# Optimization experiments

Measured on AMD Instinct MI355X. Metric: run time of the kernel, lower is better.

The kernel has to match this reference:

```python
import jax, jax.numpy as jnp
import numpy as np

RX = 49
R = 1.0
ANGLES = [-10.0, 0.0, 10.0]


def _make_kernels(rx, r, angles_deg):
    # same construction as the torch __init__
    angles = np.rad2deg(np.arctan(r * np.tan(np.deg2rad(np.asarray(angles_deg, np.float64)))))
    ks = []
    for A in angles:
        lval = np.arange(rx) - rx // 2
        lval = np.round(lval * np.tan(np.deg2rad(A))).astype(np.int32)
        ry = (lval.max() - lval.min()) // 2 * 2 + 1
        i, _ = np.meshgrid(np.arange(ry), np.arange(rx))
        i = i - ry // 2
        k = (i == lval[:, None]).astype(np.float32)[None, None]  # [1,1,rx,ry], one nonzero per row
        ks.append(k)
    return ks

_KERNELS = [jnp.asarray(k) for k in _make_kernels(RX, R, ANGLES)]
_PADS = [(int(k.shape[2]) // 2, int(k.shape[3]) // 2) for k in _KERNELS]  # (pc, pr)


def _boxfilter(x, k, pc, pr):
    # torch.conv2d(F.pad(x,(pr,pr,pc,pc)), k) == cross-correlation with symmetric zero pad
    return jax.lax.conv_general_dilated(x, k, (1, 1), ((pc, pc), (pr, pr)),
                                        dimension_numbers=('NCHW', 'OIHW', 'NCHW'))


def _reflect(x, size):
    # PyTorch reflection padding for align_corners=True: reflect about [0, size-1]
    span = size - 1
    if span <= 0:
        return jnp.zeros_like(x)
    ax = jnp.abs(x)
    extra = jnp.mod(ax, span)
    flips = jnp.floor(ax / span)
    out = jnp.where(jnp.mod(flips, 2.0) == 0.0, extra, span - extra)
    return jnp.clip(out, 0.0, span)


def _grid_sample(x, grid):
    # bilinear, padding_mode='reflection', align_corners=True; x:[B,C,H,W], grid:[B,Hg,Wg,2]
    B, C, H, W = x.shape
    gx = _reflect((grid[..., 0] + 1.0) * 0.5 * (W - 1), W)
    gy = _reflect((grid[..., 1] + 1.0) * 0.5 * (H - 1), H)
    x0 = jnp.floor(gx)
    y0 = jnp.floor(gy)
    wx = gx - x0
    wy = gy - y0
    xi0 = jnp.clip(x0, 0, W - 1).astype(jnp.int32)
    yi0 = jnp.clip(y0, 0, H - 1).astype(jnp.int32)
    xi1 = jnp.clip(x0 + 1.0, 0, W - 1).astype(jnp.int32)
    yi1 = jnp.clip(y0 + 1.0, 0, H - 1).astype(jnp.int32)
    gather = jax.vmap(lambda img, yi, xi: img[:, yi, xi])  # [B,C,Hg,Wg]
    v00 = gather(x, yi0, xi0)
    v01 = gather(x, yi0, xi1)
    v10 = gather(x, yi1, xi0)
    v11 = gather(x, yi1, xi1)
    wx = wx[:, None]  # [B,1,Hg,Wg] broadcast over channel
    wy = wy[:, None]
    return (v00 * (1 - wx) * (1 - wy) + v01 * wx * (1 - wy)
            + v10 * (1 - wx) * wy + v11 * wx * wy)


def setup_inputs() -> dict:
    key = jax.random.key(0)
    k1, k2, k3, k4 = jax.random.split(key, 4)
    B, H, W = 1, 2048, 2048
    X = jax.random.uniform(k1, (B, 1, H, W), jnp.float32)
    y = jax.random.uniform(k2, (B, 1, H, W), jnp.float32)
    hX = jax.random.normal(k3, (B, 1, H, W), jnp.float32)
    coor = jax.random.uniform(k4, (B, H, W, 2), jnp.float32, minval=-1.0, maxval=1.0)
    return {"X": X, "y": y, "hX": hX, "coor": coor}


def reference(X, y, hX, coor):
    # N: normalization = boxfilter of ones (computed once per shape in torch; recomputed here)
    N = [_boxfilter(jnp.ones_like(X), k, pc, pr) for k, (pc, pr) in zip(_KERNELS, _PADS)]
    X0 = X
    Xc = X
    for (k, (pc, pr)), Ni in zip(zip(_KERNELS, _PADS), N):
        b = _boxfilter(y - Xc, k, pc, pr) / Ni
        b = _boxfilter(b, k, pc, pr) / Ni
        Xc = Xc + b
    return _grid_sample(Xc - X0, coor) + hX
```

## Files before the change

kernel.cpp:

```cpp
#include <hip/hip_runtime.h>
#include <hip/hip_fp16.h>

static constexpr int HH = 2048;
static constexpr int WW = 2048;
static constexpr int PADT = 24;
static constexpr int PADL = 8;
static constexpr int SW   = WW + 2 * PADL;
static constexpr int PROWS = HH + 2 * PADT;
static constexpr size_t PadElems = (size_t)PROWS * SW;
static constexpr int RSP = 8;
static constexpr int RV = 16;

__device__ constexpr int CS[9] = {-24,-19,-14,-8,-2, 3, 9,15,20};
__device__ constexpr int CE[9] = {-20,-15, -9,-3, 2, 8,14,19,24};
__device__ constexpr int CO[9] = { -4, -3, -2,-1, 0, 1, 2, 3, 4};

union U32H2 { unsigned u; __half2 h; };
__device__ __forceinline__ __half2 u2h(unsigned u) { U32H2 x; x.u = u; return x.h; }
__device__ __forceinline__ unsigned h2u(__half2 h) { U32H2 x; x.h = h; return x.u; }

__device__ __forceinline__ void swz_s2(int& bx, int& by) {
  const int bid = blockIdx.x;
  const int xcd = bid & 7, i = bid >> 3;
  by = xcd * 32 + (i & 31);
  bx = i >> 5;
}
__device__ __forceinline__ void swz_v(int& bx, int& by) {
  const int bid = blockIdx.x;
  const int xcd = bid & 7, i = bid >> 3;
  by = xcd * 16 + (i & 15);
  bx = i >> 4;
}

template<int SS, int EE, int OO, int NROWS>
__device__ __forceinline__ void seg2p(const __half* __restrict__ tp, int h0, int w2,
                                      __half2* __restrict__ acc) {
  constexpr int NR = EE - SS;
  constexpr bool EVEN = ((OO & 1) == 0);
  const size_t st = SW / 2;
  const unsigned* p = (const unsigned*)(tp + (size_t)(h0 + SS + PADT) * SW +
                                        (w2 + PADL + (EVEN ? OO : OO - 1)));
  unsigned ring[NR];
  __half2 s = u2h(0u);
#pragma unroll
  for (int k = 0; k < NR; ++k) {
    unsigned u;
    if constexpr (EVEN) { u = p[k * st]; }
    else { const unsigned ul = p[k * st], ur = p[k * st + 1]; u = (ul >> 16) | (ur << 16); }
    ring[k] = u;
    s = __hadd2(s, u2h(u));
  }
#pragma unroll
  for (int r = 0; r < NROWS; ++r) {
    unsigned u;
    if constexpr (EVEN) { u = p[(NR + r) * st]; }
    else { const unsigned ul = p[(NR + r) * st], ur = p[(NR + r) * st + 1]; u = (ul >> 16) | (ur << 16); }
    const __half2 v = u2h(u);
    acc[r] = __hadd2(acc[r], __hadd2(s, v));
    s = __hadd2(s, __hsub2(v, u2h(ring[r % NR])));
    ring[r % NR] = u;
  }
}

template<int SGN, int NROWS>
__device__ __forceinline__ void filt_slant2p(const __half* __restrict__ tp, int h0, int w2,
                                             __half2* __restrict__ acc) {
#pragma unroll
  for (int r = 0; r < NROWS; ++r) acc[r] = u2h(0u);
  seg2p<-24, -20, -4 * SGN, NROWS>(tp, h0, w2, acc);
  seg2p<-19, -15, -3 * SGN, NROWS>(tp, h0, w2, acc);
  seg2p<-14,  -9, -2 * SGN, NROWS>(tp, h0, w2, acc);
  seg2p< -8,  -3, -1 * SGN, NROWS>(tp, h0, w2, acc);
  seg2p< -2,   2,  0      , NROWS>(tp, h0, w2, acc);
  seg2p<  3,   8,  1 * SGN, NROWS>(tp, h0, w2, acc);
  seg2p<  9,  14,  2 * SGN, NROWS>(tp, h0, w2, acc);
  seg2p< 15,  19,  3 * SGN, NROWS>(tp, h0, w2, acc);
  seg2p< 20,  24,  4 * SGN, NROWS>(tp, h0, w2, acc);
}

template<int A>
__device__ __forceinline__ float rcpcnt(int h, int w) {
  if (h >= 24 && h <= 2023 && w >= 4 && w <= 2043) return 1.0f / 49.0f;
  int cnt = 0;
  const int sgn = (A == 0) ? -1 : 1;
#pragma unroll
  for (int j = 0; j < 9; ++j) {
    const int ww = w + sgn * CO[j];
    const int ov = min(h + CE[j], HH - 1) - max(h + CS[j], 0) + 1;
    if (ww >= 0 && ww < WW && ov > 0) cnt += ov;
  }
  return 1.0f / (float)cnt;
}

__device__ __forceinline__ float rcpcnt1(int h) {
  return 1.0f / (float)(min(h + 24, HH - 1) - max(h - 24, 0) + 1);
}

template<int A>
__global__ __launch_bounds__(256) void passA(const __half* __restrict__ tcur,
                                             __half* __restrict__ bp) {
  int bx, by; swz_s2(bx, by);
  const int w2 = (bx * 256 + threadIdx.x) * 2;
  const int h0 = by * RSP;
  __half2 acc[RSP];
  filt_slant2p<(A == 0) ? -1 : 1, RSP>(tcur, h0, w2, acc);
#pragma unroll
  for (int r = 0; r < RSP; ++r) {
    const int h = h0 + r;
    const float2 f = __half22float2(acc[r]);
    *(unsigned*)(bp + (size_t)(h + PADT) * SW + (w2 + PADL)) =
        h2u(__floats2half2_rn(f.x * rcpcnt<A>(h, w2), f.y * rcpcnt<A>(h, w2 + 1)));
  }
}

template<int A>
__global__ __launch_bounds__(256) void passB(const __half* __restrict__ bp,
                                             __half* __restrict__ tcur) {
  int bx, by; swz_s2(bx, by);
  const int w2 = (bx * 256 + threadIdx.x) * 2;
  const int h0 = by * RSP;
  __half2 acc[RSP];
  filt_slant2p<(A == 0) ? -1 : 1, RSP>(bp, h0, w2, acc);
#pragma unroll
  for (int r = 0; r < RSP; ++r) {
    const int h = h0 + r;
    unsigned* o = (unsigned*)(tcur + (size_t)(h + PADT) * SW + (w2 + PADL));
    const float2 cur = __half22float2(u2h(*o));
    const float2 f = __half22float2(acc[r]);
    *o = h2u(__floats2half2_rn(cur.x - f.x * rcpcnt<A>(h, w2),
                               cur.y - f.y * rcpcnt<A>(h, w2 + 1)));
  }
}

template<int A>
__global__ __launch_bounds__(256) void passBF(const __half* __restrict__ bp,
                                              __half* __restrict__ tcur,
                                              const __half* __restrict__ t0h,
                                              unsigned int* __restrict__ scaleU) {
  int bx, by; swz_s2(bx, by);
  const int w2 = (bx * 256 + threadIdx.x) * 2;
  const int h0 = by * RSP;
  __half2 acc[RSP];
  filt_slant2p<(A == 0) ? -1 : 1, RSP>(bp, h0, w2, acc);
  float m = 0.0f;
#pragma unroll
  for (int r = 0; r < RSP; ++r) {
    const int h = h0 + r;
    const float2 t0 = __half22float2(u2h(*(const unsigned*)(t0h + (size_t)h * WW + w2)));
    unsigned* o = (unsigned*)(tcur + (size_t)(h + PADT) * SW + (w2 + PADL));
    const float2 cur = __half22float2(u2h(*o));
    const float2 f = __half22float2(acc[r]);
    const float rx = t0.x - cur.x + f.x * rcpcnt<A>(h, w2);
    const float ry = t0.y - cur.y + f.y * rcpcnt<A>(h, w2 + 1);
    *o = h2u(__floats2half2_rn(rx, ry));
    m = fmaxf(m, fmaxf(fabsf(rx), fabsf(ry)));
  }
#pragma unroll
  for (int off = 32; off >= 1; off >>= 1) m = fmaxf(m, __shfl_xor(m, off));
  __shared__ float red[4];
  if ((threadIdx.x & 63) == 0) red[threadIdx.x >> 6] = m;
  __syncthreads();
  if (threadIdx.x == 0) {
    const float bm = fmaxf(fmaxf(red[0], red[1]), fmaxf(red[2], red[3]));
    atomicMax(scaleU, __float_as_uint(bm));
  }
}

__global__ __launch_bounds__(256) void passA1v(const __half* __restrict__ tcur,
                                               __half* __restrict__ bp) {
  int bx, by; swz_v(bx, by);
  const int w2 = (bx * 256 + threadIdx.x) * 2;
  const int h0 = by * RV;
  const size_t st = SW / 2;
  const unsigned* p = (const unsigned*)(tcur + (size_t)(h0 - 24 + PADT) * SW + (w2 + PADL));
  __half2 s = u2h(0u);
#pragma unroll
  for (int k = 0; k < 48; ++k) s = __hadd2(s, u2h(p[k * st]));
#pragma unroll
  for (int r = 0; r < RV; ++r) {
    const int h = h0 + r;
    const __half2 vin = u2h(p[(48 + r) * st]);
    const float2 f = __half22float2(__hadd2(s, vin));
    const float rc = rcpcnt1(h);
    *(unsigned*)(bp + (size_t)(h + PADT) * SW + (w2 + PADL)) =
        h2u(__floats2half2_rn(f.x * rc, f.y * rc));
    s = __hadd2(s, __hsub2(vin, u2h(p[r * st])));
  }
}

__global__ __launch_bounds__(256) void passB1v(const __half* __restrict__ bp,
                                               __half* __restrict__ tcur) {
  int bx, by; swz_v(bx, by);
  const int w2 = (bx * 256 + threadIdx.x) * 2;
  const int h0 = by * RV;
  const size_t st = SW / 2;
  const unsigned* p = (const unsigned*)(bp + (size_t)(h0 - 24 + PADT) * SW + (w2 + PADL));
  __half2 s = u2h(0u);
#pragma unroll
  for (int k = 0; k < 48; ++k) s = __hadd2(s, u2h(p[k * st]));
#pragma unroll
  for (int r = 0; r < RV; ++r) {
    const int h = h0 + r;
    const __half2 vin = u2h(p[(48 + r) * st]);
    const float2 f = __half22float2(__hadd2(s, vin));
    const float rc = rcpcnt1(h);
    unsigned* o = (unsigned*)(tcur + (size_t)(h + PADT) * SW + (w2 + PADL));
    const float2 cur = __half22float2(u2h(*o));
    *o = h2u(__floats2half2_rn(cur.x - f.x * rc, cur.y - f.y * rc));
    s = __hadd2(s, __hsub2(vin, u2h(p[r * st])));
  }
}

__global__ __launch_bounds__(256) void quantV8(const __half* __restrict__ tcur,
                                               const unsigned int* __restrict__ scaleU,
                                               unsigned long long* __restrict__ V8) {
  const int i = blockIdx.x * 256 + threadIdx.x;
  const int s = i >> 10, x2 = (i & 1023) * 2;
  const float mg = __uint_as_float(*scaleU);
  const float inv = (mg > 0.0f) ? 127.0f / mg : 0.0f;
  const unsigned* base = (const unsigned*)(tcur + (size_t)(8 * s + PADT) * SW + (x2 + PADL));
  const size_t st = SW / 2;
  unsigned long long va = 0, vb = 0;
#pragma unroll
  for (int j = 0; j < 8; ++j) {
    const float2 f = __half22float2(u2h(base[(size_t)j * st]));
    const int qa = min(max((int)rintf(f.x * inv), -127), 127);
    const int qb = min(max((int)rintf(f.y * inv), -127), 127);
    va |= (unsigned long long)(unsigned char)(qa & 0xff) << (8 * j);
    vb |= (unsigned long long)(unsigned char)(qb & 0xff) << (8 * j);
  }
  unsigned long long* o = V8 + (size_t)s * WW + x2;
  o[0] = va; o[1] = vb;
}

__global__ __launch_bounds__(64) void zeropad(__half* __restrict__ tp, __half* __restrict__ bp,
                                              unsigned int* __restrict__ scaleU) {
  if (blockIdx.x == 0 && blockIdx.y == 0 && threadIdx.x == 0) *scaleU = 0u;
  __half* buf = blockIdx.y ? bp : tp;
  const int row = blockIdx.x;
  __half* r = buf + (size_t)row * SW;
  const __half z = __float2half(0.0f);
  if (row < PADT || row >= PADT + HH) {
    for (int c = threadIdx.x; c < SW; c += 64) r[c] = z;
  } else if (threadIdx.x < PADL) {
    r[threadIdx.x] = z;
    r[PADL + WW + threadIdx.x] = z;
  }
}

__global__ __launch_bounds__(256) void sub2pad(const float* __restrict__ y,
                                               const float* __restrict__ X,
                                               __half* __restrict__ tcur,
                                               __half* __restrict__ t0h) {
  const int i = blockIdx.x * 256 + threadIdx.x;
  const int p = i * 4;
  const int h = p >> 11, w = p & (WW - 1);
  const float4 Y = ((const float4*)y)[i];
  const float4 Xv = ((const float4*)X)[i];
  union { __half2 h2; unsigned u; } a, b;
  a.h2 = __floats2half2_rn(Y.x - Xv.x, Y.y - Xv.y);
  b.h2 = __floats2half2_rn(Y.z - Xv.z, Y.w - Xv.w);
  uint2 o; o.x = a.u; o.y = b.u;
  *(uint2*)(tcur + (size_t)(h + PADT) * SW + (w + PADL)) = o;
  *(uint2*)(t0h + (size_t)p) = o;
}

__global__ __launch_bounds__(256) void gather_k(const unsigned long long* __restrict__ V8,
                                                const unsigned int* __restrict__ scaleU,
                                                const unsigned long long* __restrict__ coorU,
                                                const float* __restrict__ hX,
                                                float* __restrict__ out) {
  const int i = blockIdx.x * 256 + threadIdx.x;
  const unsigned long long cu = __builtin_nontemporal_load(&coorU[i]);
  union { unsigned long long u; float f[2]; } cc; cc.u = cu;
  const float gx = fminf(fmaxf((cc.f[0] + 1.0f) * 0.5f * (float)(WW - 1), 0.0f), (float)(WW - 1));
  const float gy = fminf(fmaxf((cc.f[1] + 1.0f) * 0.5f * (float)(HH - 1), 0.0f), (float)(HH - 1));
  const float x0 = floorf(gx), y0 = floorf(gy);
  const float wx = gx - x0, wy = gy - y0;
  const int xi0 = min(max((int)x0, 0), WW - 1);
  const int xi1 = min(xi0 + 1, WW - 1);
  const int yi0 = min(max((int)y0, 0), HH - 1);
  const int yi1 = min(max((int)(y0 + 1.0f), 0), HH - 1);
  const int s0 = yi0 >> 3, s1 = yi1 >> 3;
  const int j0 = (yi0 & 7) * 8, j1 = (yi1 & 7) * 8;
  const unsigned long long c00 = V8[(size_t)s0 * WW + xi0];
  const unsigned long long c01 = V8[(size_t)s0 * WW + xi1];
  unsigned long long c10 = c00, c11 = c01;
  if (s1 != s0) {
    c10 = V8[(size_t)s1 * WW + xi0];
    c11 = V8[(size_t)s1 * WW + xi1];
  }
  const float v00 = (float)(signed char)(c00 >> j0);
  const float v01 = (float)(signed char)(c01 >> j0);
  const float v10 = (float)(signed char)(c10 >> j1);
  const float v11 = (float)(signed char)(c11 >> j1);
  const float sc = __uint_as_float(*scaleU) * (1.0f / 127.0f);
  const float hx = __builtin_nontemporal_load(&hX[i]);
  const float bil = v00 * (1.0f - wx) * (1.0f - wy) + v01 * wx * (1.0f - wy) +
                    v10 * (1.0f - wx) * wy + v11 * wx * wy;
  __builtin_nontemporal_store(bil * sc + hx, &out[i]);
}

extern "C" void kernel_launch(void* const* d_in, const int* in_sizes, int n_in,
                              void* d_out, int out_size, void* d_ws, size_t ws_size,
                              hipStream_t stream) {
  const float* X    = (const float*)d_in[0];
  const float* y    = (const float*)d_in[1];
  const float* hX   = (const float*)d_in[2];
  const float* coor = (const float*)d_in[3];
  float* out = (float*)d_out;

  __half* tcur = (__half*)d_ws;
  __half* bp   = tcur + PadElems;
  __half* t0h  = bp + PadElems;
  unsigned long long* V8 = (unsigned long long*)(t0h + (size_t)HH * WW);
  unsigned int* scaleU = (unsigned int*)(V8 + (size_t)(HH / 8) * WW);

  const int n = HH * WW;
  const int sblocks = (WW / 512) * (HH / RSP);
  const int vblocks = (WW / 512) * (HH / RV);

  zeropad<<<dim3(PROWS, 2, 1), 64, 0, stream>>>(tcur, bp, scaleU);
  sub2pad<<<(n / 4) / 256, 256, 0, stream>>>(y, X, tcur, t0h);

  passA<0><<<sblocks, 256, 0, stream>>>(tcur, bp);
  passB<0><<<sblocks, 256, 0, stream>>>(bp, tcur);
  passA1v<<<vblocks, 256, 0, stream>>>(tcur, bp);
  passB1v<<<vblocks, 256, 0, stream>>>(bp, tcur);
  passA<2><<<sblocks, 256, 0, stream>>>(tcur, bp);
  passBF<2><<<sblocks, 256, 0, stream>>>(bp, tcur, t0h, scaleU);

  quantV8<<<((HH / 8) * (WW / 2)) / 256, 256, 0, stream>>>(tcur, scaleU, V8);
  gather_k<<<n / 256, 256, 0, stream>>>(V8, scaleU, (const unsigned long long*)coor, hX, out);
}
```

Measured before the change: 147.3 us.

## Use overlapping 7-row int8 packs so bilinear gather needs two loads

```diff
diff --git a/kernel.cpp b/kernel.cpp
--- a/kernel.cpp
+++ b/kernel.cpp
@@ -8,8 +8,9 @@
 static constexpr int SW   = WW + 2 * PADL;
 static constexpr int PROWS = HH + 2 * PADT;
 static constexpr size_t PadElems = (size_t)PROWS * SW;
-static constexpr int RSP = 8;
+static constexpr int RSP = 16;
 static constexpr int RV = 16;
+static constexpr int NG = 293;
 
 __device__ constexpr int CS[9] = {-24,-19,-14,-8,-2, 3, 9,15,20};
 __device__ constexpr int CE[9] = {-20,-15, -9,-3, 2, 8,14,19,24};
@@ -19,13 +20,7 @@
 __device__ __forceinline__ __half2 u2h(unsigned u) { U32H2 x; x.u = u; return x.h; }
 __device__ __forceinline__ unsigned h2u(__half2 h) { U32H2 x; x.h = h; return x.u; }
 
-__device__ __forceinline__ void swz_s2(int& bx, int& by) {
-  const int bid = blockIdx.x;
-  const int xcd = bid & 7, i = bid >> 3;
-  by = xcd * 32 + (i & 31);
-  bx = i >> 5;
-}
-__device__ __forceinline__ void swz_v(int& bx, int& by) {
+__device__ __forceinline__ void swz_f(int& bx, int& by) {
   const int bid = blockIdx.x;
   const int xcd = bid & 7, i = bid >> 3;
   by = xcd * 16 + (i & 15);
@@ -99,7 +94,7 @@
 template<int A>
 __global__ __launch_bounds__(256) void passA(const __half* __restrict__ tcur,
                                              __half* __restrict__ bp) {
-  int bx, by; swz_s2(bx, by);
+  int bx, by; swz_f(bx, by);
   const int w2 = (bx * 256 + threadIdx.x) * 2;
   const int h0 = by * RSP;
   __half2 acc[RSP];
@@ -116,7 +111,7 @@
 template<int A>
 __global__ __launch_bounds__(256) void passB(const __half* __restrict__ bp,
                                              __half* __restrict__ tcur) {
-  int bx, by; swz_s2(bx, by);
+  int bx, by; swz_f(bx, by);
   const int w2 = (bx * 256 + threadIdx.x) * 2;
   const int h0 = by * RSP;
   __half2 acc[RSP];
@@ -137,7 +132,7 @@
                                               __half* __restrict__ tcur,
                                               const __half* __restrict__ t0h,
                                               unsigned int* __restrict__ scaleU) {
-  int bx, by; swz_s2(bx, by);
+  int bx, by; swz_f(bx, by);
   const int w2 = (bx * 256 + threadIdx.x) * 2;
   const int h0 = by * RSP;
   __half2 acc[RSP];
@@ -168,7 +163,7 @@
 
 __global__ __launch_bounds__(256) void passA1v(const __half* __restrict__ tcur,
                                                __half* __restrict__ bp) {
-  int bx, by; swz_v(bx, by);
+  int bx, by; swz_f(bx, by);
   const int w2 = (bx * 256 + threadIdx.x) * 2;
   const int h0 = by * RV;
   const size_t st = SW / 2;
@@ -190,7 +185,7 @@
 
 __global__ __launch_bounds__(256) void passB1v(const __half* __restrict__ bp,
                                                __half* __restrict__ tcur) {
-  int bx, by; swz_v(bx, by);
+  int bx, by; swz_f(bx, by);
   const int w2 = (bx * 256 + threadIdx.x) * 2;
   const int h0 = by * RV;
   const size_t st = SW / 2;
@@ -211,14 +206,14 @@
   }
 }
 
-__global__ __launch_bounds__(256) void quantV8(const __half* __restrict__ tcur,
-                                               const unsigned int* __restrict__ scaleU,
-                                               unsigned long long* __restrict__ V8) {
+__global__ __launch_bounds__(256) void quantV8s7(const __half* __restrict__ tcur,
+                                                 const unsigned int* __restrict__ scaleU,
+                                                 unsigned long long* __restrict__ V8) {
   const int i = blockIdx.x * 256 + threadIdx.x;
   const int s = i >> 10, x2 = (i & 1023) * 2;
   const float mg = __uint_as_float(*scaleU);
   const float inv = (mg > 0.0f) ? 127.0f / mg : 0.0f;
-  const unsigned* base = (const unsigned*)(tcur + (size_t)(8 * s + PADT) * SW + (x2 + PADL));
+  const unsigned* base = (const unsigned*)(tcur + (size_t)(7 * s + PADT) * SW + (x2 + PADL));
   const size_t st = SW / 2;
   unsigned long long va = 0, vb = 0;
 #pragma unroll
@@ -233,36 +228,38 @@
   o[0] = va; o[1] = vb;
 }
 
-__global__ __launch_bounds__(64) void zeropad(__half* __restrict__ tp, __half* __restrict__ bp,
-                                              unsigned int* __restrict__ scaleU) {
-  if (blockIdx.x == 0 && blockIdx.y == 0 && threadIdx.x == 0) *scaleU = 0u;
-  __half* buf = blockIdx.y ? bp : tp;
-  const int row = blockIdx.x;
-  __half* r = buf + (size_t)row * SW;
-  const __half z = __float2half(0.0f);
-  if (row < PADT || row >= PADT + HH) {
-    for (int c = threadIdx.x; c < SW; c += 64) r[c] = z;
-  } else if (threadIdx.x < PADL) {
-    r[threadIdx.x] = z;
-    r[PADL + WW + threadIdx.x] = z;
-  }
-}
-
-__global__ __launch_bounds__(256) void sub2pad(const float* __restrict__ y,
-                                               const float* __restrict__ X,
-                                               __half* __restrict__ tcur,
-                                               __half* __restrict__ t0h) {
-  const int i = blockIdx.x * 256 + threadIdx.x;
-  const int p = i * 4;
-  const int h = p >> 11, w = p & (WW - 1);
-  const float4 Y = ((const float4*)y)[i];
-  const float4 Xv = ((const float4*)X)[i];
-  union { __half2 h2; unsigned u; } a, b;
-  a.h2 = __floats2half2_rn(Y.x - Xv.x, Y.y - Xv.y);
-  b.h2 = __floats2half2_rn(Y.z - Xv.z, Y.w - Xv.w);
-  uint2 o; o.x = a.u; o.y = b.u;
-  *(uint2*)(tcur + (size_t)(h + PADT) * SW + (w + PADL)) = o;
-  *(uint2*)(t0h + (size_t)p) = o;
+__global__ __launch_bounds__(256) void initk(const float* __restrict__ y,
+                                             const float* __restrict__ X,
+                                             __half* __restrict__ tcur,
+                                             __half* __restrict__ t0h,
+                                             __half* __restrict__ bp,
+                                             unsigned int* __restrict__ scaleU) {
+  const int b = blockIdx.x;
+  if (b < 4096) {
+    const int i = b * 256 + threadIdx.x;
+    const int p = i * 4;
+    const int h = p >> 11, w = p & (WW - 1);
+    const float4 Y = ((const float4*)y)[i];
+    const float4 Xv = ((const float4*)X)[i];
+    union { __half2 h2; unsigned u; } a, c;
+    a.h2 = __floats2half2_rn(Y.x - Xv.x, Y.y - Xv.y);
+    c.h2 = __floats2half2_rn(Y.z - Xv.z, Y.w - Xv.w);
+    uint2 o; o.x = a.u; o.y = c.u;
+    *(uint2*)(tcur + (size_t)(h + PADT) * SW + (w + PADL)) = o;
+    *(uint2*)(t0h + (size_t)p) = o;
+  } else {
+    const int row = b - 4096;
+    if (row == 0 && threadIdx.x == 0) *scaleU = 0u;
+    __half* rt = tcur + (size_t)row * SW;
+    __half* rb = bp + (size_t)row * SW;
+    const __half z = __float2half(0.0f);
+    if (row < PADT || row >= PADT + HH) {
+      for (int c = threadIdx.x; c < SW; c += 256) { rt[c] = z; rb[c] = z; }
+    } else if (threadIdx.x < 2 * PADL) {
+      const int c = (threadIdx.x < PADL) ? threadIdx.x : (PADL + WW + threadIdx.x - PADL);
+      rt[c] = z; rb[c] = z;
+    }
+  }
 }
 
 __global__ __launch_bounds__(256) void gather_k(const unsigned long long* __restrict__ V8,
@@ -280,20 +277,14 @@
   const int xi0 = min(max((int)x0, 0), WW - 1);
   const int xi1 = min(xi0 + 1, WW - 1);
   const int yi0 = min(max((int)y0, 0), HH - 1);
-  const int yi1 = min(max((int)(y0 + 1.0f), 0), HH - 1);
-  const int s0 = yi0 >> 3, s1 = yi1 >> 3;
-  const int j0 = (yi0 & 7) * 8, j1 = (yi1 & 7) * 8;
-  const unsigned long long c00 = V8[(size_t)s0 * WW + xi0];
-  const unsigned long long c01 = V8[(size_t)s0 * WW + xi1];
-  unsigned long long c10 = c00, c11 = c01;
-  if (s1 != s0) {
-    c10 = V8[(size_t)s1 * WW + xi0];
-    c11 = V8[(size_t)s1 * WW + xi1];
-  }
-  const float v00 = (float)(signed char)(c00 >> j0);
-  const float v01 = (float)(signed char)(c01 >> j0);
-  const float v10 = (float)(signed char)(c10 >> j1);
-  const float v11 = (float)(signed char)(c11 >> j1);
+  const int s0 = (yi0 * 9363) >> 16;
+  const int j0 = (yi0 - s0 * 7) * 8;
+  const unsigned long long c0 = V8[(size_t)s0 * WW + xi0];
+  const unsigned long long c1 = V8[(size_t)s0 * WW + xi1];
+  const float v00 = (float)(signed char)(c0 >> j0);
+  const float v10 = (float)(signed char)(c0 >> (j0 + 8));
+  const float v01 = (float)(signed char)(c1 >> j0);
+  const float v11 = (float)(signed char)(c1 >> (j0 + 8));
   const float sc = __uint_as_float(*scaleU) * (1.0f / 127.0f);
   const float hx = __builtin_nontemporal_load(&hX[i]);
   const float bil = v00 * (1.0f - wx) * (1.0f - wy) + v01 * wx * (1.0f - wy) +
@@ -314,22 +305,21 @@
   __half* bp   = tcur + PadElems;
   __half* t0h  = bp + PadElems;
   unsigned long long* V8 = (unsigned long long*)(t0h + (size_t)HH * WW);
-  unsigned int* scaleU = (unsigned int*)(V8 + (size_t)(HH / 8) * WW);
+  unsigned int* scaleU = (unsigned int*)(V8 + (size_t)NG * WW);
 
   const int n = HH * WW;
-  const int sblocks = (WW / 512) * (HH / RSP);
-  const int vblocks = (WW / 512) * (HH / RV);
-
-  zeropad<<<dim3(PROWS, 2, 1), 64, 0, stream>>>(tcur, bp, scaleU);
-  sub2pad<<<(n / 4) / 256, 256, 0, stream>>>(y, X, tcur, t0h);
-
-  passA<0><<<sblocks, 256, 0, stream>>>(tcur, bp);
-  passB<0><<<sblocks, 256, 0, stream>>>(bp, tcur);
-  passA1v<<<vblocks, 256, 0, stream>>>(tcur, bp);
-  passB1v<<<vblocks, 256, 0, stream>>>(bp, tcur);
-  passA<2><<<sblocks, 256, 0, stream>>>(tcur, bp);
-  passBF<2><<<sblocks, 256, 0, stream>>>(bp, tcur, t0h, scaleU);
-
-  quantV8<<<((HH / 8) * (WW / 2)) / 256, 256, 0, stream>>>(tcur, scaleU, V8);
+  const int fblocks = (WW / 512) * (HH / RSP);
+  const int qblocks = (NG * (WW / 2)) / 256;
+
+  initk<<<4096 + PROWS, 256, 0, stream>>>(y, X, tcur, t0h, bp, scaleU);
+
+  passA<0><<<fblocks, 256, 0, stream>>>(tcur, bp);
+  passB<0><<<fblocks, 256, 0, stream>>>(bp, tcur);
+  passA1v<<<fblocks, 256, 0, stream>>>(tcur, bp);
+  passB1v<<<fblocks, 256, 0, stream>>>(bp, tcur);
+  passA<2><<<fblocks, 256, 0, stream>>>(tcur, bp);
+  passBF<2><<<fblocks, 256, 0, stream>>>(bp, tcur, t0h, scaleU);
+
+  quantV8s7<<<qblocks, 256, 0, stream>>>(tcur, scaleU, V8);
   gather_k<<<n / 256, 256, 0, stream>>>(V8, scaleU, (const unsigned long long*)coor, hX, out);
 }
```

After: 146.6 us. Within noise of the previous version (-0.5%).
